# Performance work log

Hardware: AMD Instinct MI355X
Metric: run time of the kernel (lower is better)

Reference implementation:

```python
import jax, jax.numpy as jnp
import numpy as np

NEAR, FAR, N_SAMPLES = 1.0, 6.0, 64
FAR_APPEND = 1000.0


def setup_inputs() -> dict:
    key = jax.random.key(0)
    ks = jax.random.split(key, 8)
    B, R = 2, 4096
    # pixel coords in a 128x128 image
    x_pix = jax.random.uniform(ks[0], (B, R, 2), dtype=jnp.float32) * 128.0
    # plausible pinhole intrinsics (fx=fy=128, cx=cy=64)
    K = jnp.array([[128.0, 0.0, 64.0], [0.0, 128.0, 64.0], [0.0, 0.0, 1.0]], dtype=jnp.float32)
    intrinsics = jnp.tile(K[None], (B, 1, 1))
    # identity rotation, small translation cam2world
    c2w = jnp.eye(4, dtype=jnp.float32).at[:3, 3].set(jnp.array([0.1, -0.2, 0.5]))
    cam2world = jnp.tile(c2w[None], (B, 1, 1))
    H = 256
    W1 = jax.random.normal(ks[1], (3, H), dtype=jnp.float32) / np.sqrt(3.0)
    b1 = jnp.zeros((H,), jnp.float32)
    W2 = jax.random.normal(ks[2], (H, H), dtype=jnp.float32) / np.sqrt(H)
    b2 = jnp.zeros((H,), jnp.float32)
    W3 = jax.random.normal(ks[3], (H, 4), dtype=jnp.float32) / np.sqrt(H)
    b3 = jnp.zeros((4,), jnp.float32)
    return {"x_pix": x_pix, "intrinsics": intrinsics, "cam2world": cam2world,
            "W1": W1, "b1": b1, "W2": W2, "b2": b2, "W3": W3, "b3": b3}


def _radiance_field(pts, W1, b1, W2, b2, W3, b3):
    # pts: (B, N, 3) -> sigma (B, N, 1), rad (B, N, 3)
    h = jax.nn.relu(pts @ W1 + b1)
    h = jax.nn.relu(h @ W2 + b2)
    o = h @ W3 + b3
    return jax.nn.relu(o[..., :1]), jax.nn.sigmoid(o[..., 1:])


def _get_world_rays(x_pix, intrinsics, cam2world):
    B, R, _ = x_pix.shape
    inv_K = jnp.linalg.inv(intrinsics)  # (B,3,3)
    xy_hom = jnp.concatenate([x_pix, jnp.ones((B, R, 1), x_pix.dtype)], axis=-1)  # (B,R,3)
    dirs_cam = jnp.einsum("bij,brj->bri", inv_K, xy_hom)  # unnormalized cam-frame dirs
    dirs_hom = jnp.concatenate([dirs_cam, jnp.zeros((B, R, 1), x_pix.dtype)], axis=-1)  # w=0 vector
    dirs_world = jnp.einsum("bij,brj->bri", cam2world, dirs_hom)[..., :3]
    origins = jnp.broadcast_to(cam2world[:, None, :3, 3], (B, R, 3))
    return origins, dirs_world


def _volume_integral(z_vals, sigmas, radiances):
    # z_vals: (S,); sigmas: (B,R,S,1); radiances: (B,R,S,3)
    dists = jnp.diff(z_vals, append=jnp.array([FAR_APPEND], z_vals.dtype))  # (S,)
    alpha = 1.0 - jnp.exp(-sigmas * dists[None, None, :, None])  # (B,R,S,1)
    Ts = jnp.cumprod(1.0 - alpha, axis=2)  # inclusive cumprod, matching torch
    weights = alpha * Ts  # (B,R,S,1)
    rgb = jnp.sum(weights * radiances, axis=2)  # (B,R,3)
    depth_map = jnp.einsum("brsv,s->brv", weights, z_vals)  # (B,R,1)
    return rgb, depth_map, weights


def reference(x_pix, intrinsics, cam2world, W1, b1, W2, b2, W3, b3):
    B, R = x_pix.shape[0], x_pix.shape[1]
    ros, rds = _get_world_rays(x_pix, intrinsics, cam2world)
    z_vals = jnp.linspace(NEAR, FAR, N_SAMPLES, dtype=x_pix.dtype)  # (S,)
    pts = ros[:, :, None, :] + rds[:, :, None, :] * z_vals[None, None, :, None]  # (B,R,S,3)
    pts = pts.reshape(B, -1, 3)
    sigma, rad = _radiance_field(pts, W1, b1, W2, b2, W3, b3)
    sigma = sigma.reshape(B, R, N_SAMPLES, 1)
    rad = rad.reshape(B, R, N_SAMPLES, 3)
    rgb, depth_map, weights = _volume_integral(z_vals, sigma, rad)
    accum = jnp.sum(weights, axis=-2)  # (B,R,1)
    rgb = rgb + (1.0 - accum)  # white background
    return rgb, depth_map
```

## Files before the change

kernel.cpp:

```cpp
#include <hip/hip_runtime.h>

typedef unsigned short u16;
typedef _Float16 f16x8 __attribute__((ext_vector_type(8)));
typedef float    f32x4 __attribute__((ext_vector_type(4)));

#define NRAYS 8192

#define WS_W2T  0
#define WS_B2   131072
#define WS_W3   132096
#define WS_B3   136192
#define WS_W1   136208
#define WS_B1   139280
#define WS_INTR 140304
#define WS_C2W  140384

__device__ __forceinline__ float bf2f(u16 u){
  union { unsigned int i; float f; } v; v.i = ((unsigned int)u) << 16; return v.f;
}
__device__ __forceinline__ u16 f2h(float f){
  union { _Float16 h; u16 u; } v; v.h = (_Float16)f;
  return v.u;
}
__device__ __forceinline__ int detect_bf16(const void* intr){
  return (((const u16*)intr)[0] == 0x4300u) ? 1 : 0;
}

__device__ __forceinline__ void conv_arr(const void* src, float* dst, int n, int bf, int tid){
  if (bf){
    const u16* s = (const u16*)src;
    for (int i = tid; i < n; i += 256) dst[i] = bf2f(s[i]);
  } else {
    const float* s = (const float*)src;
    for (int i = tid; i < n; i += 256) dst[i] = s[i];
  }
}

__global__ void prep(const void* __restrict__ W2, const void* __restrict__ W1,
                     const void* __restrict__ b1, const void* __restrict__ b2,
                     const void* __restrict__ W3, const void* __restrict__ b3,
                     const void* __restrict__ intr, const void* __restrict__ c2w,
                     char* __restrict__ ws)
{
  const int bf = detect_bf16(intr);
  const int t = threadIdx.x;
  if (blockIdx.x == 16){
    conv_arr(W1,  (float*)(ws + WS_W1),  768,  bf, t);
    conv_arr(b1,  (float*)(ws + WS_B1),  256,  bf, t);
    conv_arr(b2,  (float*)(ws + WS_B2),  256,  bf, t);
    conv_arr(W3,  (float*)(ws + WS_W3),  1024, bf, t);
    conv_arr(b3,  (float*)(ws + WS_B3),  4,    bf, t);
    conv_arr(intr,(float*)(ws + WS_INTR),18,   bf, t);
    conv_arr(c2w, (float*)(ws + WS_C2W), 32,   bf, t);
    return;
  }
  __shared__ u16 tile[64][72];
  const int bx = blockIdx.x & 3;
  const int by = blockIdx.x >> 2;
  const int c = t & 63, rb = t >> 6;
  u16* W2T = (u16*)(ws + WS_W2T);
  #pragma unroll
  for (int rr = 0; rr < 64; rr += 4){
    int k = bx*64 + rr + rb;
    int n = by*64 + c;
    float v = bf ? bf2f(((const u16*)W2)[k*256 + n]) : ((const float*)W2)[k*256 + n];
    tile[rr + rb][c] = f2h(v);
  }
  __syncthreads();
  #pragma unroll
  for (int rr = 0; rr < 64; rr += 4){
    int n = by*64 + rr + rb;
    int k = bx*64 + c;
    W2T[n*256 + k] = tile[c][rr + rb];
  }
}

__global__ __launch_bounds__(256, 2) void nerf_fused(
    const void* __restrict__ x_pix,
    const void* __restrict__ intr,
    const char* __restrict__ ws,
    float* __restrict__ out)
{
  __shared__ __align__(16) u16 h1s[128 * 256];

  const int tid = threadIdx.x;
  const int l   = tid & 63;
  const int w   = tid >> 6;
  const int ray = w >> 1;
  const int rayg = blockIdx.x * 2 + ray;
  const int bb   = rayg >> 12;
  const int bf   = detect_bf16(intr);

  const float* intrf = (const float*)(ws + WS_INTR);
  const float* c2wf  = (const float*)(ws + WS_C2W);
  const float* W1f   = (const float*)(ws + WS_W1);
  const float* b1f   = (const float*)(ws + WS_B1);
  const float* b2f   = (const float*)(ws + WS_B2);
  const float* W3f   = (const float*)(ws + WS_W3);
  const float* b3f   = (const float*)(ws + WS_B3);
  const u16*   W2T   = (const u16*)(ws + WS_W2T);

  float px, py;
  if (bf){
    px = bf2f(((const u16*)x_pix)[rayg*2 + 0]);
    py = bf2f(((const u16*)x_pix)[rayg*2 + 1]);
  } else {
    px = ((const float*)x_pix)[rayg*2 + 0];
    py = ((const float*)x_pix)[rayg*2 + 1];
  }
  float Ka[9], Mm[16];
  #pragma unroll
  for (int i = 0; i < 9;  i++) Ka[i] = intrf[bb*9  + i];
  #pragma unroll
  for (int i = 0; i < 16; i++) Mm[i] = c2wf[bb*16 + i];
  float a = Ka[0], b_ = Ka[1], c = Ka[2];
  float d = Ka[3], e  = Ka[4], f = Ka[5];
  float g = Ka[6], h  = Ka[7], i9 = Ka[8];
  float det = a*(e*i9 - f*h) - b_*(d*i9 - f*g) + c*(d*h - e*g);
  float inv = 1.0f / det;
  float i00 = (e*i9 - f*h)*inv, i01 = (c*h - b_*i9)*inv, i02 = (b_*f - c*e)*inv;
  float i10 = (f*g - d*i9)*inv, i11 = (a*i9 - c*g)*inv, i12 = (c*d - a*f)*inv;
  float i20 = (d*h - e*g)*inv,  i21 = (b_*g - a*h)*inv, i22 = (a*e - b_*d)*inv;
  float dcx = i00*px + i01*py + i02;
  float dcy = i10*px + i11*py + i12;
  float dcz = i20*px + i21*py + i22;
  float dx = Mm[0]*dcx + Mm[1]*dcy + Mm[2]*dcz;
  float dy = Mm[4]*dcx + Mm[5]*dcy + Mm[6]*dcz;
  float dz = Mm[8]*dcx + Mm[9]*dcy + Mm[10]*dcz;
  float ox = Mm[3], oy = Mm[7], oz = Mm[11];

  const int kbase = (w & 1)*128 + l*2;
  float aa0, aa1, gg0, gg1;
  {
    float2 r0 = *(const float2*)(W1f + kbase);
    float2 r1 = *(const float2*)(W1f + 256 + kbase);
    float2 r2 = *(const float2*)(W1f + 512 + kbase);
    float2 rb = *(const float2*)(b1f + kbase);
    aa0 = ox*r0.x + oy*r1.x + oz*r2.x + rb.x;
    aa1 = ox*r0.y + oy*r1.y + oz*r2.y + rb.y;
    gg0 = dx*r0.x + dy*r1.x + dz*r2.x;
    gg1 = dx*r0.y + dy*r1.y + dz*r2.y;
  }
  const float step = 5.0f / 63.0f;
  const int chunk_w = ((w & 1) << 4) + (l >> 2);
  const int sub_b   = (l & 3) << 2;
  {
    char* hb = (char*)h1s + (ray*64)*512;
    #pragma unroll 8
    for (int s = 0; s < 64; s++){
      float z = 1.0f + step * (float)s;
      u16 e0 = f2h(fmaxf(fmaf(gg0, z, aa0), 0.0f));
      u16 e1 = f2h(fmaxf(fmaf(gg1, z, aa1), 0.0f));
      unsigned pk = (unsigned)e0 | ((unsigned)e1 << 16);
      *(unsigned*)(hb + s*512 + ((chunk_w ^ (s & 7)) << 4) + sub_b) = pk;
    }
  }
  __syncthreads();

  const int col = l & 15;
  const int q   = l >> 4;
  const int c7  = col & 7;
  const int nbase = w * 64;

  f32x4 acc[4][8];
  #pragma unroll
  for (int nt = 0; nt < 4; nt++)
    #pragma unroll
    for (int mt = 0; mt < 8; mt++)
      acc[nt][mt] = (f32x4){0.f, 0.f, 0.f, 0.f};

  const u16* Ab = W2T + (nbase + col)*256 + q*8;
  f16x8 afc[4];
  #pragma unroll
  for (int nt = 0; nt < 4; nt++)
    afc[nt] = *(const f16x8*)(Ab + nt*16*256);

  const char* hbase = (const char*)h1s;
  #pragma unroll
  for (int kc = 0; kc < 8; kc++){
    f16x8 afn[4];
    if (kc < 7){
      #pragma unroll
      for (int nt = 0; nt < 4; nt++)
        afn[nt] = *(const f16x8*)(Ab + nt*16*256 + (kc+1)*32);
    }
    f16x8 bfr[8];
    const int swz = ((kc*4 + q) ^ c7) << 4;
    #pragma unroll
    for (int mt = 0; mt < 8; mt++)
      bfr[mt] = *(const f16x8*)(hbase + (mt*16 + col)*512 + swz);
    #pragma unroll
    for (int nt = 0; nt < 4; nt++)
      #pragma unroll
      for (int mt = 0; mt < 8; mt++)
        acc[nt][mt] = __builtin_amdgcn_mfma_f32_16x16x32_f16(
            afc[nt], bfr[mt], acc[nt][mt], 0, 0, 0);
    if (kc < 7){
      #pragma unroll
      for (int nt = 0; nt < 4; nt++)
        afc[nt] = afn[nt];
    }
  }

  f32x4 o4[8];
  #pragma unroll
  for (int mt = 0; mt < 8; mt++) o4[mt] = (f32x4){0.f, 0.f, 0.f, 0.f};

  #pragma unroll
  for (int nt = 0; nt < 4; nt++){
    const int n2 = nbase + nt*16 + q*4;
    f32x4 b2v  = *(const f32x4*)(b2f + n2);
    f32x4 w3r0 = *(const f32x4*)(W3f + n2*4);
    f32x4 w3r1 = *(const f32x4*)(W3f + (n2+1)*4);
    f32x4 w3r2 = *(const f32x4*)(W3f + (n2+2)*4);
    f32x4 w3r3 = *(const f32x4*)(W3f + (n2+3)*4);
    #pragma unroll
    for (int mt = 0; mt < 8; mt++){
      f32x4 t = acc[nt][mt] + b2v;
      f32x4 hv;
      hv.x = fmaxf(t.x, 0.0f); hv.y = fmaxf(t.y, 0.0f);
      hv.z = fmaxf(t.z, 0.0f); hv.w = fmaxf(t.w, 0.0f);
      o4[mt] = o4[mt] + hv.x*w3r0 + hv.y*w3r1 + hv.z*w3r2 + hv.w*w3r3;
    }
  }

  #pragma unroll
  for (int mt = 0; mt < 8; mt++)
    #pragma unroll
    for (int cc = 0; cc < 4; cc++){
      float v = o4[mt][cc];
      v += __shfl_xor(v, 16, 64);
      v += __shfl_xor(v, 32, 64);
      o4[mt][cc] = v;
    }

  __syncthreads();
  f32x4* obuf = (f32x4*)h1s;
  if (q == 0){
    #pragma unroll
    for (int mt = 0; mt < 8; mt++)
      obuf[w*128 + mt*16 + col] = o4[mt];
  }
  __syncthreads();

  if (w < 2){
    const int m = w*64 + l;
    f32x4 oj = obuf[m] + obuf[128 + m] + obuf[256 + m] + obuf[384 + m];
    f32x4 b3v = *(const f32x4*)b3f;
    float o_s0 = oj.x + b3v.x;
    float o_s1 = oj.y + b3v.y;
    float o_s2 = oj.z + b3v.z;
    float o_s3 = oj.w + b3v.w;

    const float zc    = 1.0f + step * (float)l;
    const float znext = (l == 63) ? 1000.0f : (1.0f + step * (float)(l + 1));
    const float dist  = znext - zc;
    float sigma = fmaxf(o_s0, 0.0f);
    float alpha = 1.0f - __expf(-sigma * dist);
    float t = 1.0f - alpha;
    #pragma unroll
    for (int sh = 1; sh < 64; sh <<= 1){
      float u = __shfl_up(t, sh, 64);
      if (l >= sh) t *= u;
    }
    float wgt = alpha * t;
    float r0 = 1.0f / (1.0f + __expf(-o_s1));
    float r1 = 1.0f / (1.0f + __expf(-o_s2));
    float r2 = 1.0f / (1.0f + __expf(-o_s3));
    float s0 = wgt*r0, s1 = wgt*r1, s2 = wgt*r2, sw = wgt, sz = wgt*zc;
    #pragma unroll
    for (int sh = 1; sh < 64; sh <<= 1){
      s0 += __shfl_xor(s0, sh, 64);
      s1 += __shfl_xor(s1, sh, 64);
      s2 += __shfl_xor(s2, sh, 64);
      sw += __shfl_xor(sw, sh, 64);
      sz += __shfl_xor(sz, sh, 64);
    }
    if (l == 0){
      const int rg = blockIdx.x*2 + w;
      float bg = 1.0f - sw;
      out[rg*3 + 0] = s0 + bg;
      out[rg*3 + 1] = s1 + bg;
      out[rg*3 + 2] = s2 + bg;
      out[3*NRAYS + rg] = sz;
    }
  }
}

extern "C" void kernel_launch(void* const* d_in, const int* in_sizes, int n_in,
                              void* d_out, int out_size, void* d_ws, size_t ws_size,
                              hipStream_t stream)
{
  const void* x_pix = d_in[0];
  const void* intr  = d_in[1];
  const void* c2w   = d_in[2];
  const void* W1    = d_in[3];
  const void* b1    = d_in[4];
  const void* W2    = d_in[5];
  const void* b2    = d_in[6];
  const void* W3    = d_in[7];
  const void* b3    = d_in[8];
  float* outp = (float*)d_out;
  char*  ws   = (char*)d_ws;

  hipLaunchKernelGGL(prep, dim3(17), dim3(256), 0, stream,
                     W2, W1, b1, b2, W3, b3, intr, c2w, ws);
  hipLaunchKernelGGL(nerf_fused, dim3(NRAYS/2), dim3(256), 0, stream,
                     x_pix, intr, ws, outp);
}
```

Measured before the change: 177.7 us.

## Compute output layer with MFMA via LDS-staged fp16 hidden activations

The layer-3 projection (256->4) moves from per-lane FP32 FMAs plus cross-lane shuffles and a four-way LDS reduction to MFMA. The relu'd layer-2 activations are written back to shared memory as fp16 and multiplied by a transposed fp16 copy of W3 prepared in the prep kernel. The LDS B-fragments of the layer-2 GEMM are also double-buffered so their loads overlap the current k-chunk's MFMAs. This adds another LDS round trip, two extra barriers and more registers, and rounds the layer-3 input to fp16.

```diff
diff --git a/kernel.cpp b/kernel.cpp
--- a/kernel.cpp
+++ b/kernel.cpp
@@ -2,13 +2,14 @@
 
 typedef unsigned short u16;
 typedef _Float16 f16x8 __attribute__((ext_vector_type(8)));
+typedef _Float16 f16x4 __attribute__((ext_vector_type(4)));
 typedef float    f32x4 __attribute__((ext_vector_type(4)));
 
 #define NRAYS 8192
 
 #define WS_W2T  0
 #define WS_B2   131072
-#define WS_W3   132096
+#define WS_W3PT 132096
 #define WS_B3   136192
 #define WS_W1   136208
 #define WS_B1   139280
@@ -48,10 +49,17 @@
     conv_arr(W1,  (float*)(ws + WS_W1),  768,  bf, t);
     conv_arr(b1,  (float*)(ws + WS_B1),  256,  bf, t);
     conv_arr(b2,  (float*)(ws + WS_B2),  256,  bf, t);
-    conv_arr(W3,  (float*)(ws + WS_W3),  1024, bf, t);
     conv_arr(b3,  (float*)(ws + WS_B3),  4,    bf, t);
     conv_arr(intr,(float*)(ws + WS_INTR),18,   bf, t);
     conv_arr(c2w, (float*)(ws + WS_C2W), 32,   bf, t);
+    {
+      u16* w3p = (u16*)(ws + WS_W3PT);
+      for (int i = t; i < 1024; i += 256){
+        int j = i >> 8, k = i & 255;
+        float v = bf ? bf2f(((const u16*)W3)[k*4 + j]) : ((const float*)W3)[k*4 + j];
+        w3p[i] = f2h(v);
+      }
+    }
     return;
   }
   __shared__ u16 tile[64][72];
@@ -82,6 +90,7 @@
     float* __restrict__ out)
 {
   __shared__ __align__(16) u16 h1s[128 * 256];
+  __shared__ __align__(16) float obuf[128 * 4];
 
   const int tid = threadIdx.x;
   const int l   = tid & 63;
@@ -96,8 +105,7 @@
   const float* W1f   = (const float*)(ws + WS_W1);
   const float* b1f   = (const float*)(ws + WS_B1);
   const float* b2f   = (const float*)(ws + WS_B2);
-  const float* W3f   = (const float*)(ws + WS_W3);
-  const float* b3f   = (const float*)(ws + WS_B3);
+  const u16*   W3pT  = (const u16*)(ws + WS_W3PT);
   const u16*   W2T   = (const u16*)(ws + WS_W2T);
 
   float px, py;
@@ -170,83 +178,100 @@
       acc[nt][mt] = (f32x4){0.f, 0.f, 0.f, 0.f};
 
   const u16* Ab = W2T + (nbase + col)*256 + q*8;
-  f16x8 afc[4];
+  const char* hbase = (const char*)h1s;
+
+  f16x8 afc[4], bfc[8];
   #pragma unroll
   for (int nt = 0; nt < 4; nt++)
     afc[nt] = *(const f16x8*)(Ab + nt*16*256);
-
-  const char* hbase = (const char*)h1s;
+  {
+    const int swz = (q ^ c7) << 4;
+    #pragma unroll
+    for (int mt = 0; mt < 8; mt++)
+      bfc[mt] = *(const f16x8*)(hbase + (mt*16 + col)*512 + swz);
+  }
+
   #pragma unroll
   for (int kc = 0; kc < 8; kc++){
-    f16x8 afn[4];
+    f16x8 afn[4], bfn[8];
     if (kc < 7){
       #pragma unroll
       for (int nt = 0; nt < 4; nt++)
         afn[nt] = *(const f16x8*)(Ab + nt*16*256 + (kc+1)*32);
-    }
-    f16x8 bfr[8];
-    const int swz = ((kc*4 + q) ^ c7) << 4;
-    #pragma unroll
-    for (int mt = 0; mt < 8; mt++)
-      bfr[mt] = *(const f16x8*)(hbase + (mt*16 + col)*512 + swz);
+      const int swz = (((kc+1)*4 + q) ^ c7) << 4;
+      #pragma unroll
+      for (int mt = 0; mt < 8; mt++)
+        bfn[mt] = *(const f16x8*)(hbase + (mt*16 + col)*512 + swz);
+    }
     #pragma unroll
     for (int nt = 0; nt < 4; nt++)
       #pragma unroll
       for (int mt = 0; mt < 8; mt++)
         acc[nt][mt] = __builtin_amdgcn_mfma_f32_16x16x32_f16(
-            afc[nt], bfr[mt], acc[nt][mt], 0, 0, 0);
+            afc[nt], bfc[mt], acc[nt][mt], 0, 0, 0);
     if (kc < 7){
       #pragma unroll
-      for (int nt = 0; nt < 4; nt++)
-        afc[nt] = afn[nt];
-    }
-  }
-
-  f32x4 o4[8];
-  #pragma unroll
-  for (int mt = 0; mt < 8; mt++) o4[mt] = (f32x4){0.f, 0.f, 0.f, 0.f};
-
+      for (int nt = 0; nt < 4; nt++) afc[nt] = afn[nt];
+      #pragma unroll
+      for (int mt = 0; mt < 8; mt++) bfc[mt] = bfn[mt];
+    }
+  }
+
+  f16x8 w3frag[8];
+  {
+    const u16* wp = W3pT + (col & 3)*256 + q*8;
+    #pragma unroll
+    for (int kc = 0; kc < 8; kc++)
+      w3frag[kc] = *(const f16x8*)(wp + kc*32);
+  }
+
+  __syncthreads();
   #pragma unroll
   for (int nt = 0; nt < 4; nt++){
     const int n2 = nbase + nt*16 + q*4;
-    f32x4 b2v  = *(const f32x4*)(b2f + n2);
-    f32x4 w3r0 = *(const f32x4*)(W3f + n2*4);
-    f32x4 w3r1 = *(const f32x4*)(W3f + (n2+1)*4);
-    f32x4 w3r2 = *(const f32x4*)(W3f + (n2+2)*4);
-    f32x4 w3r3 = *(const f32x4*)(W3f + (n2+3)*4);
+    const int chb = n2 >> 3;
+    const int sub = (n2 & 7) * 2;
+    f32x4 b2v = *(const f32x4*)(b2f + n2);
     #pragma unroll
     for (int mt = 0; mt < 8; mt++){
+      const int m = mt*16 + col;
       f32x4 t = acc[nt][mt] + b2v;
-      f32x4 hv;
-      hv.x = fmaxf(t.x, 0.0f); hv.y = fmaxf(t.y, 0.0f);
-      hv.z = fmaxf(t.z, 0.0f); hv.w = fmaxf(t.w, 0.0f);
-      o4[mt] = o4[mt] + hv.x*w3r0 + hv.y*w3r1 + hv.z*w3r2 + hv.w*w3r3;
-    }
-  }
-
-  #pragma unroll
-  for (int mt = 0; mt < 8; mt++)
-    #pragma unroll
-    for (int cc = 0; cc < 4; cc++){
-      float v = o4[mt][cc];
-      v += __shfl_xor(v, 16, 64);
-      v += __shfl_xor(v, 32, 64);
-      o4[mt][cc] = v;
-    }
-
-  __syncthreads();
-  f32x4* obuf = (f32x4*)h1s;
-  if (q == 0){
-    #pragma unroll
-    for (int mt = 0; mt < 8; mt++)
-      obuf[w*128 + mt*16 + col] = o4[mt];
+      f16x4 hq;
+      hq.x = (_Float16)fmaxf(t.x, 0.0f);
+      hq.y = (_Float16)fmaxf(t.y, 0.0f);
+      hq.z = (_Float16)fmaxf(t.z, 0.0f);
+      hq.w = (_Float16)fmaxf(t.w, 0.0f);
+      *(f16x4*)((char*)h1s + m*512 + ((chb ^ (m & 7)) << 4) + sub) = hq;
+    }
+  }
+  __syncthreads();
+
+  f32x4 acc3[2];
+  acc3[0] = (f32x4){0.f,0.f,0.f,0.f};
+  acc3[1] = (f32x4){0.f,0.f,0.f,0.f};
+  #pragma unroll
+  for (int mt3 = 0; mt3 < 2; mt3++){
+    const int mrow = w*32 + mt3*16 + col;
+    const int m7 = mrow & 7;
+    #pragma unroll
+    for (int kc = 0; kc < 8; kc++){
+      f16x8 a3 = *(const f16x8*)((const char*)h1s + mrow*512 + (((kc*4 + q) ^ m7) << 4));
+      acc3[mt3] = __builtin_amdgcn_mfma_f32_16x16x32_f16(a3, w3frag[kc], acc3[mt3], 0, 0, 0);
+    }
+  }
+  if (col < 4){
+    #pragma unroll
+    for (int mt3 = 0; mt3 < 2; mt3++)
+      #pragma unroll
+      for (int rr = 0; rr < 4; rr++)
+        obuf[(w*32 + mt3*16 + q*4 + rr)*4 + col] = acc3[mt3][rr];
   }
   __syncthreads();
 
   if (w < 2){
     const int m = w*64 + l;
-    f32x4 oj = obuf[m] + obuf[128 + m] + obuf[256 + m] + obuf[384 + m];
-    f32x4 b3v = *(const f32x4*)b3f;
+    f32x4 oj  = *(const f32x4*)&obuf[m*4];
+    f32x4 b3v = *(const f32x4*)(ws + WS_B3);
     float o_s0 = oj.x + b3v.x;
     float o_s1 = oj.y + b3v.y;
     float o_s2 = oj.z + b3v.z;
```

Measured after the change: 183.1 us. +3.1%, slower.
